# Performance work log

Measured on AMD Instinct MI355X. Metric: run time of the kernel, lower is better.

The kernel has to match this reference:

```python
import jax, jax.numpy as jnp
import numpy as np

IMAGE_SIZE = 224
BLUR_SIGMA = 4.0  # PIL ImageFilter.GaussianBlur(radius=4): radius acts as std dev
BLUR_RADIUS = 8   # truncate kernel at 2*sigma


def _gaussian_blur(x, sigma=BLUR_SIGMA, radius=BLUR_RADIUS):
    # separable gaussian blur on NCHW, SAME padding
    t = jnp.arange(-radius, radius + 1, dtype=x.dtype)
    kern = jnp.exp(-0.5 * (t / sigma) ** 2)
    kern = kern / kern.sum()
    dn = ('NCHW', 'OIHW', 'NCHW')
    x = jax.lax.conv_general_dilated(x, kern.reshape(1, 1, 1, -1), (1, 1), 'SAME', dimension_numbers=dn)
    x = jax.lax.conv_general_dilated(x, kern.reshape(1, 1, -1, 1), (1, 1), 'SAME', dimension_numbers=dn)
    return x


def setup_inputs() -> dict:
    key = jax.random.key(0)
    ks = jax.random.split(key, 8)
    N = 1000
    inp = {
        'z': jax.random.normal(ks[0], (1, 512), jnp.float32),
        'fmap0': jax.random.normal(ks[1], (1, 64, 56, 56), jnp.float32),
        'fmap1': jax.random.normal(ks[2], (1, 128, 28, 28), jnp.float32),
        'fmap2': jax.random.normal(ks[3], (1, 256, 14, 14), jnp.float32),
        'z_lib': jax.random.normal(ks[4], (N, 512), jnp.float32),
        'lib0': jax.random.normal(ks[5], (N, 64, 56, 56), jnp.float32),
        'lib1': jax.random.normal(ks[6], (N, 128, 28, 28), jnp.float32),
        'lib2': jax.random.normal(ks[7], (N, 256, 14, 14), jnp.float32),
        'k': 5,
    }
    return inp


def reference(z, fmap0, fmap1, fmap2, z_lib, lib0, lib1, lib2, k):
    # distances = ||z_lib - z||_2 over feature dim -> [N]
    dists = jnp.linalg.norm(z_lib - z, axis=1)
    # topk smallest
    neg_vals, indices = jax.lax.top_k(-dists, k)
    z_score = (-neg_vals).mean()

    s_total = jnp.zeros((1, 1, IMAGE_SIZE, IMAGE_SIZE), jnp.float32)
    for fmap, lib in ((fmap0, lib0), (fmap1, lib1), (fmap2, lib2)):
        nearest = lib[indices]                            # [k, C, H, W]
        s = jnp.linalg.norm(nearest - fmap, axis=1)        # [k, H, W] (channel-wise L2)
        s = s.min(axis=0, keepdims=True)                   # [1, H, W]
        s_up = jax.image.resize(s[None], (1, 1, IMAGE_SIZE, IMAGE_SIZE), method='bilinear')
        s_total = s_total + s_up
    s_total = _gaussian_blur(s_total)
    return z_score, s_total
```

## Files before the change

### kernel.cpp

```cpp
#include <hip/hip_runtime.h>
#include <hip/hip_bf16.h>
#include <math.h>

#define IMG 224
#define NLIB 1000
#define ZD 512
#define MAXK 8
#define NTHR 512
#define STHR 256


__device__ __forceinline__ int clampk(int k) {
    if (k < 1) k = 1;
    if (k > MAXK) k = MAXK;
    return k;
}

__global__ void __launch_bounds__(NTHR) k_dist(const float* __restrict__ z,
                                               const float* __restrict__ zlib,
                                               float* __restrict__ dists) {
    int lane = threadIdx.x & 63, wave = threadIdx.x >> 6;
    int gw = blockIdx.x * (NTHR / 64) + wave;
    if (gw >= NLIB) return;
    const float4* row4 = (const float4*)(zlib + (size_t)gw * ZD);
    const float4* z4   = (const float4*)z;
    float4 a0 = row4[lane],      b0 = z4[lane];
    float4 a1 = row4[64 + lane], b1 = z4[64 + lane];
    float acc = 0.f, d;
    d = a0.x - b0.x; acc += d * d;  d = a0.y - b0.y; acc += d * d;
    d = a0.z - b0.z; acc += d * d;  d = a0.w - b0.w; acc += d * d;
    d = a1.x - b1.x; acc += d * d;  d = a1.y - b1.y; acc += d * d;
    d = a1.z - b1.z; acc += d * d;  d = a1.w - b1.w; acc += d * d;
#pragma unroll
    for (int off = 32; off > 0; off >>= 1) acc += __shfl_xor(acc, off, 64);
    if (lane == 0) dists[gw] = sqrtf(acc);
}

__global__ void __launch_bounds__(STHR) k_score(
        const float* __restrict__ f0, const float* __restrict__ f1,
        const float* __restrict__ f2,
        const float* __restrict__ l0, const float* __restrict__ l1,
        const float* __restrict__ l2,
        const float* __restrict__ dists, const int* __restrict__ kp,
        float* __restrict__ out,
        float* __restrict__ s0, float* __restrict__ s1, float* __restrict__ s2) {

    __shared__ int idxs[MAXK];
    int tid = threadIdx.x;
    int lane = tid & 63, wave = tid >> 6;
    int k = clampk(*kp);

    if (wave == 0) {
        float vals[16];
#pragma unroll
        for (int j = 0; j < 16; ++j) {
            int e = lane + 64 * j;
            vals[j] = (e < NLIB) ? dists[e] : 3.4e38f;
        }
        float ssum = 0.f;
        for (int it = 0; it < k; ++it) {
            float bv = 3.4e38f; int bi = 0x7fffffff;
#pragma unroll
            for (int j = 0; j < 16; ++j) {
                if (vals[j] < bv) { bv = vals[j]; bi = lane + 64 * j; }
            }
#pragma unroll
            for (int off = 1; off < 64; off <<= 1) {
                float ov = __shfl_xor(bv, off, 64);
                int   oi = __shfl_xor(bi, off, 64);
                if (ov < bv || (ov == bv && oi < bi)) { bv = ov; bi = oi; }
            }
#pragma unroll
            for (int j = 0; j < 16; ++j) {
                if (lane + 64 * j == bi) vals[j] = 3.4e38f;
            }
            if (lane == 0) { idxs[it] = bi; ssum += bv; }
        }
        if (lane == 0 && blockIdx.x == 0) out[0] = ssum / (float)k;
    }
    __syncthreads();

    int j = blockIdx.x * STHR + tid;
    int n0 = k * 3136, n1 = k * 1568, n2 = k * 784;
    if (j >= n0 + n1 + n2) return;

    const float* fmp; const float* lbp; float* op;
    int kk, p, cbase, HW, Cfull;
    if (j < n0) {
        kk = j / 3136; p = j % 3136; cbase = 0;
        HW = 3136; Cfull = 64; fmp = f0; lbp = l0;
        op = s0 + kk * 3136 + p;
    } else if (j < n0 + n1) {
        int r = j - n0; kk = r / 1568; int q = r % 1568;
        int part = q / 784; p = q % 784; cbase = part * 64;
        HW = 784; Cfull = 128; fmp = f1; lbp = l1;
        op = s1 + part * (MAXK * 784) + kk * 784 + p;
    } else {
        int r = j - n0 - n1; kk = r / 784; int q = r % 784;
        int part = q / 196; p = q % 196; cbase = part * 64;
        HW = 196; Cfull = 256; fmp = f2; lbp = l2;
        op = s2 + part * (MAXK * 196) + kk * 196 + p;
    }

    const float* le = lbp + (size_t)idxs[kk] * (size_t)Cfull * HW + (size_t)cbase * HW + p;
    const float* fe = fmp + (size_t)cbase * HW + p;
    float acc = 0.f;
#pragma unroll 8
    for (int c = 0; c < 64; ++c) {
        float d = le[(size_t)c * HW] - fe[(size_t)c * HW];
        acc += d * d;
    }
    *op = acc;
}

__device__ __forceinline__ float bilin(const float* __restrict__ msm, int Wl, int Win,
                                       int bx, int by, float scl, int gx, int gy) {
    float sxf = ((float)gx + 0.5f) * scl - 0.5f;
    float syf = ((float)gy + 0.5f) * scl - 0.5f;
    float fx = floorf(sxf), fy = floorf(syf);
    float wx = sxf - fx,    wy = syf - fy;
    int ix = (int)fx, iy = (int)fy;
    int x0c = min(max(ix, 0), Win - 1) - bx, x1c = min(max(ix + 1, 0), Win - 1) - bx;
    int y0c = min(max(iy, 0), Win - 1) - by, y1c = min(max(iy + 1, 0), Win - 1) - by;
    float v00 = msm[y0c * Wl + x0c], v10 = msm[y0c * Wl + x1c];
    float v01 = msm[y1c * Wl + x0c], v11 = msm[y1c * Wl + x1c];
    return (1.f - wy) * ((1.f - wx) * v00 + wx * v10) +
           wy * ((1.f - wx) * v01 + wx * v11);
}

__global__ void __launch_bounds__(NTHR) k_tile(
        const float* __restrict__ s0, const float* __restrict__ s1,
        const float* __restrict__ s2, const int* __restrict__ kp,
        float* __restrict__ out) {

    __shared__ float msm0[100];
    __shared__ float msm1[36];
    __shared__ float msm2[9];
    __shared__ float pre[32 * 32];
    __shared__ float mid[32 * 16];
    __shared__ float wk[17];

    int tid = threadIdx.x;
    int k = clampk(*kp);
    int tx = blockIdx.x % 14, ty = blockIdx.x / 14;
    int x0 = tx * 16, y0 = ty * 16;
    int b0x = x0 / 4 - 3,  b0y = y0 / 4 - 3;
    int b1x = x0 / 8 - 2,  b1y = y0 / 8 - 2;
    int b2x = x0 / 16 - 1, b2y = y0 / 16 - 1;

    if (tid < 17) {
        float r = (float)(tid - 8) * 0.25f;
        wk[tid] = expf(-0.5f * r * r);
    }

    if (tid >= 32 && tid < 32 + 145) {
        int i = tid - 32;
        float m = 3.4e38f;
        if (i < 100) {
            int ly = i / 10, lx = i % 10;
            int gx = min(max(b0x + lx, 0), 55), gy = min(max(b0y + ly, 0), 55);
            int p = gy * 56 + gx;
            for (int kk = 0; kk < k; ++kk) m = fminf(m, s0[kk * 3136 + p]);
            msm0[i] = sqrtf(m);
        } else if (i < 136) {
            int r = i - 100; int ly = r / 6, lx = r % 6;
            int gx = min(max(b1x + lx, 0), 27), gy = min(max(b1y + ly, 0), 27);
            int p = gy * 28 + gx;
            for (int kk = 0; kk < k; ++kk) {
                float v = s1[kk * 784 + p] + s1[MAXK * 784 + kk * 784 + p];
                m = fminf(m, v);
            }
            msm1[r] = sqrtf(m);
        } else {
            int r = i - 136; int ly = r / 3, lx = r % 3;
            int gx = min(max(b2x + lx, 0), 13), gy = min(max(b2y + ly, 0), 13);
            int p = gy * 14 + gx;
            for (int kk = 0; kk < k; ++kk) {
                float v = s2[kk * 196 + p] + s2[MAXK * 196 + kk * 196 + p]
                        + s2[2 * MAXK * 196 + kk * 196 + p] + s2[3 * MAXK * 196 + kk * 196 + p];
                m = fminf(m, v);
            }
            msm2[r] = sqrtf(m);
        }
    }
    __syncthreads();

    float wsum = 0.f;
#pragma unroll
    for (int t = 0; t < 17; ++t) wsum += wk[t];
    float inv2 = 1.f / (wsum * wsum);

    for (int i = tid; i < 32 * 32; i += NTHR) {
        int lx = i % 32, ly = i / 32;
        int gx = x0 - 8 + lx, gy = y0 - 8 + ly;
        float v = 0.f;
        if ((unsigned)gx < (unsigned)IMG && (unsigned)gy < (unsigned)IMG) {
            v = bilin(msm0, 10, 56, b0x, b0y, 0.25f,   gx, gy)
              + bilin(msm1, 6,  28, b1x, b1y, 0.125f,  gx, gy)
              + bilin(msm2, 3,  14, b2x, b2y, 0.0625f, gx, gy);
        }
        pre[i] = v;
    }
    __syncthreads();

    {
        int i = tid;
        if (i < 32 * 16) {
            int cx = i % 16, ly = i / 16;
            float acc = 0.f;
#pragma unroll
            for (int t = 0; t < 17; ++t) acc += wk[t] * pre[ly * 32 + cx + t];
            mid[ly * 16 + cx] = acc;
        }
    }
    __syncthreads();

    if (tid < 16 * 16) {
        int ox = tid % 16, oy = tid / 16;
        float acc = 0.f;
#pragma unroll
        for (int t = 0; t < 17; ++t) acc += wk[t] * mid[(oy + t) * 16 + ox];
        out[1 + (y0 + oy) * IMG + (x0 + ox)] = acc * inv2;
    }
}

extern "C" void kernel_launch(void* const* d_in, const int* in_sizes, int n_in,
                              void* d_out, int out_size, void* d_ws, size_t ws_size,
                              hipStream_t stream) {
    const float* z    = (const float*)d_in[0];
    const float* f0   = (const float*)d_in[1];
    const float* f1   = (const float*)d_in[2];
    const float* f2   = (const float*)d_in[3];
    const float* zlib = (const float*)d_in[4];
    const float* l0   = (const float*)d_in[5];
    const float* l1   = (const float*)d_in[6];
    const float* l2   = (const float*)d_in[7];
    const int*   kp   = (const int*)d_in[8];
    float* out = (float*)d_out;

    float* ws    = (float*)d_ws;
    float* dists = ws;
    float* s0    = ws + 1024;
    float* s1    = s0 + MAXK * 3136;
    float* s2    = s1 + 2 * MAXK * 784;

    k_dist<<<(NLIB + 7) / 8, NTHR, 0, stream>>>(z, zlib, dists);

    int njobs = MAXK * (3136 + 1568 + 784);
    k_score<<<(njobs + STHR - 1) / STHR, STHR, 0, stream>>>(
        f0, f1, f2, l0, l1, l2, dists, kp, out, s0, s1, s2);

    k_tile<<<196, NTHR, 0, stream>>>(s0, s1, s2, kp, out);
}
```

Measured before the change: 24.26 us.

## Vectorize score loads with float4, split channels finer, per-wave top-k

Each score thread now handles four adjacent pixels through float4 loads over 32 channels, and the channel reduction is split into more partial sums (2/4/8 parts per level) that the tile kernel adds back together. Each active wave computes top-k itself and keeps only its own index, so the block-wide barrier and shared index array are gone. The aim is fewer memory instructions, wider coalesced loads and no block barrier, at the cost of repeating the top-k work in every wave and more partial-sum reads in the tile kernel.

New measurement: 25.57 us. 5.4% more time.

```diff
diff --git a/kernel.cpp b/kernel.cpp
--- a/kernel.cpp
+++ b/kernel.cpp
@@ -45,24 +45,52 @@
         float* __restrict__ out,
         float* __restrict__ s0, float* __restrict__ s1, float* __restrict__ s2) {
 
-    __shared__ int idxs[MAXK];
     int tid = threadIdx.x;
     int lane = tid & 63, wave = tid >> 6;
     int k = clampk(*kp);
 
-    if (wave == 0) {
+    int n0 = k * 1568, n1 = k * 784, n2 = k * 392;
+    int njobs = n0 + n1 + n2;
+    int j = blockIdx.x * STHR + tid;
+
+    const float* fmp = nullptr; const float* lbp = nullptr; float* op = nullptr;
+    int kk = 0, pq = 0, cbase = 0, HW = 0, Cfull = 0;
+    bool valid = (j < njobs);
+    if (valid) {
+        if (j < n0) {
+            int r = j;           kk = r / 1568; int q = r % 1568;
+            int part = q / 784;  pq = q % 784;  cbase = part * 32;
+            HW = 3136; Cfull = 64;  fmp = f0; lbp = l0;
+            op = s0 + part * (MAXK * 3136) + kk * 3136;
+        } else if (j < n0 + n1) {
+            int r = j - n0;      kk = r / 784;  int q = r % 784;
+            int part = q / 196;  pq = q % 196;  cbase = part * 32;
+            HW = 784;  Cfull = 128; fmp = f1; lbp = l1;
+            op = s1 + part * (MAXK * 784) + kk * 784;
+        } else {
+            int r = j - n0 - n1; kk = r / 392;  int q = r % 392;
+            int part = q / 49;   pq = q % 49;   cbase = part * 32;
+            HW = 196;  Cfull = 256; fmp = f2; lbp = l2;
+            op = s2 + part * (MAXK * 196) + kk * 196;
+        }
+    }
+
+    int waveBase = blockIdx.x * STHR + wave * 64;
+    bool dotopk = (waveBase < njobs) || (blockIdx.x == 0 && wave == 0);
+    int myidx = 0;
+    if (dotopk) {
         float vals[16];
 #pragma unroll
-        for (int j = 0; j < 16; ++j) {
-            int e = lane + 64 * j;
-            vals[j] = (e < NLIB) ? dists[e] : 3.4e38f;
+        for (int q = 0; q < 16; ++q) {
+            int e = lane + 64 * q;
+            vals[q] = (e < NLIB) ? dists[e] : 3.4e38f;
         }
         float ssum = 0.f;
         for (int it = 0; it < k; ++it) {
             float bv = 3.4e38f; int bi = 0x7fffffff;
 #pragma unroll
-            for (int j = 0; j < 16; ++j) {
-                if (vals[j] < bv) { bv = vals[j]; bi = lane + 64 * j; }
+            for (int q = 0; q < 16; ++q) {
+                if (vals[q] < bv) { bv = vals[q]; bi = lane + 64 * q; }
             }
 #pragma unroll
             for (int off = 1; off < 64; off <<= 1) {
@@ -71,46 +99,31 @@
                 if (ov < bv || (ov == bv && oi < bi)) { bv = ov; bi = oi; }
             }
 #pragma unroll
-            for (int j = 0; j < 16; ++j) {
-                if (lane + 64 * j == bi) vals[j] = 3.4e38f;
-            }
-            if (lane == 0) { idxs[it] = bi; ssum += bv; }
-        }
-        if (lane == 0 && blockIdx.x == 0) out[0] = ssum / (float)k;
-    }
-    __syncthreads();
-
-    int j = blockIdx.x * STHR + tid;
-    int n0 = k * 3136, n1 = k * 1568, n2 = k * 784;
-    if (j >= n0 + n1 + n2) return;
-
-    const float* fmp; const float* lbp; float* op;
-    int kk, p, cbase, HW, Cfull;
-    if (j < n0) {
-        kk = j / 3136; p = j % 3136; cbase = 0;
-        HW = 3136; Cfull = 64; fmp = f0; lbp = l0;
-        op = s0 + kk * 3136 + p;
-    } else if (j < n0 + n1) {
-        int r = j - n0; kk = r / 1568; int q = r % 1568;
-        int part = q / 784; p = q % 784; cbase = part * 64;
-        HW = 784; Cfull = 128; fmp = f1; lbp = l1;
-        op = s1 + part * (MAXK * 784) + kk * 784 + p;
-    } else {
-        int r = j - n0 - n1; kk = r / 784; int q = r % 784;
-        int part = q / 196; p = q % 196; cbase = part * 64;
-        HW = 196; Cfull = 256; fmp = f2; lbp = l2;
-        op = s2 + part * (MAXK * 196) + kk * 196 + p;
-    }
-
-    const float* le = lbp + (size_t)idxs[kk] * (size_t)Cfull * HW + (size_t)cbase * HW + p;
-    const float* fe = fmp + (size_t)cbase * HW + p;
-    float acc = 0.f;
-#pragma unroll 8
-    for (int c = 0; c < 64; ++c) {
-        float d = le[(size_t)c * HW] - fe[(size_t)c * HW];
-        acc += d * d;
-    }
-    *op = acc;
+            for (int q = 0; q < 16; ++q) {
+                if (lane + 64 * q == bi) vals[q] = 3.4e38f;
+            }
+            if (it == kk) myidx = bi;
+            ssum += bv;
+        }
+        if (blockIdx.x == 0 && tid == 0) out[0] = ssum / (float)k;
+    }
+
+    if (!valid) return;
+
+    const float4* lb4 = (const float4*)(lbp + (size_t)myidx * (size_t)Cfull * HW
+                                            + (size_t)cbase * HW);
+    const float4* fb4 = (const float4*)(fmp + (size_t)cbase * HW);
+    int HW4 = HW >> 2;
+    float ax = 0.f, ay = 0.f, az = 0.f, aw = 0.f;
+#pragma unroll
+    for (int c = 0; c < 32; ++c) {
+        float4 a = lb4[c * HW4 + pq];
+        float4 b = fb4[c * HW4 + pq];
+        float dx = a.x - b.x, dy = a.y - b.y, dz = a.z - b.z, dw = a.w - b.w;
+        ax += dx * dx; ay += dy * dy; az += dz * dz; aw += dw * dw;
+    }
+    float4 r; r.x = ax; r.y = ay; r.z = az; r.w = aw;
+    ((float4*)op)[pq] = r;
 }
 
 __device__ __forceinline__ float bilin(const float* __restrict__ msm, int Wl, int Win,
@@ -153,21 +166,27 @@
         wk[tid] = expf(-0.5f * r * r);
     }
 
-    if (tid >= 32 && tid < 32 + 145) {
-        int i = tid - 32;
+    if (tid >= 64 && tid < 64 + 145) {
+        int i = tid - 64;
         float m = 3.4e38f;
         if (i < 100) {
             int ly = i / 10, lx = i % 10;
             int gx = min(max(b0x + lx, 0), 55), gy = min(max(b0y + ly, 0), 55);
             int p = gy * 56 + gx;
-            for (int kk = 0; kk < k; ++kk) m = fminf(m, s0[kk * 3136 + p]);
+            for (int kk = 0; kk < k; ++kk) {
+                float v = s0[kk * 3136 + p] + s0[MAXK * 3136 + kk * 3136 + p];
+                m = fminf(m, v);
+            }
             msm0[i] = sqrtf(m);
         } else if (i < 136) {
             int r = i - 100; int ly = r / 6, lx = r % 6;
             int gx = min(max(b1x + lx, 0), 27), gy = min(max(b1y + ly, 0), 27);
             int p = gy * 28 + gx;
             for (int kk = 0; kk < k; ++kk) {
-                float v = s1[kk * 784 + p] + s1[MAXK * 784 + kk * 784 + p];
+                float v = 0.f;
+#pragma unroll
+                for (int part = 0; part < 4; ++part)
+                    v += s1[part * (MAXK * 784) + kk * 784 + p];
                 m = fminf(m, v);
             }
             msm1[r] = sqrtf(m);
@@ -176,8 +195,10 @@
             int gx = min(max(b2x + lx, 0), 13), gy = min(max(b2y + ly, 0), 13);
             int p = gy * 14 + gx;
             for (int kk = 0; kk < k; ++kk) {
-                float v = s2[kk * 196 + p] + s2[MAXK * 196 + kk * 196 + p]
-                        + s2[2 * MAXK * 196 + kk * 196 + p] + s2[3 * MAXK * 196 + kk * 196 + p];
+                float v = 0.f;
+#pragma unroll
+                for (int part = 0; part < 8; ++part)
+                    v += s2[part * (MAXK * 196) + kk * 196 + p];
                 m = fminf(m, v);
             }
             msm2[r] = sqrtf(m);
@@ -203,15 +224,12 @@
     }
     __syncthreads();
 
-    {
-        int i = tid;
-        if (i < 32 * 16) {
-            int cx = i % 16, ly = i / 16;
-            float acc = 0.f;
-#pragma unroll
-            for (int t = 0; t < 17; ++t) acc += wk[t] * pre[ly * 32 + cx + t];
-            mid[ly * 16 + cx] = acc;
-        }
+    if (tid < 32 * 16) {
+        int cx = tid % 16, ly = tid / 16;
+        float acc = 0.f;
+#pragma unroll
+        for (int t = 0; t < 17; ++t) acc += wk[t] * pre[ly * 32 + cx + t];
+        mid[ly * 16 + cx] = acc;
     }
     __syncthreads();
 
@@ -241,12 +259,12 @@
     float* ws    = (float*)d_ws;
     float* dists = ws;
     float* s0    = ws + 1024;
-    float* s1    = s0 + MAXK * 3136;
-    float* s2    = s1 + 2 * MAXK * 784;
+    float* s1    = s0 + 2 * MAXK * 3136;
+    float* s2    = s1 + 4 * MAXK * 784;
 
     k_dist<<<(NLIB + 7) / 8, NTHR, 0, stream>>>(z, zlib, dists);
 
-    int njobs = MAXK * (3136 + 1568 + 784);
+    int njobs = MAXK * (1568 + 784 + 392);
     k_score<<<(njobs + STHR - 1) / STHR, STHR, 0, stream>>>(
         f0, f1, f2, l0, l1, l2, dists, kp, out, s0, s1, s2);
 
```
